# Kernel tuning notes

Measured on AMD Instinct MI355X. Metric: run time of the kernel, lower is better.

## Reference

```python
import jax, jax.numpy as jnp
import numpy as np

EMBED_DIM = 1024

def setup_inputs() -> dict:
    key = jax.random.key(0)
    kx, kq, kk, kv = jax.random.split(key, 4)
    scale = 1.0 / np.sqrt(EMBED_DIM)  # Kaiming-uniform-ish init scale
    x = jax.random.normal(kx, (4, 2048, EMBED_DIM), dtype=jnp.float32)
    Wq = jax.random.uniform(kq, (EMBED_DIM, EMBED_DIM), jnp.float32, -scale, scale)
    Wk = jax.random.uniform(kk, (EMBED_DIM, EMBED_DIM), jnp.float32, -scale, scale)
    Wv = jax.random.uniform(kv, (EMBED_DIM, EMBED_DIM), jnp.float32, -scale, scale)
    return {"x": x, "Wq": Wq, "Wk": Wk, "Wv": Wv}

def reference(x, Wq, Wk, Wv):
    # Linear layers: y = x @ W.T (torch nn.Linear convention, no bias)
    q = jnp.einsum('bsd,ed->bse', x, Wq)
    k = jnp.einsum('bsd,ed->bse', x, Wk)
    v = jnp.einsum('bsd,ed->bse', x, Wv)
    d = k.shape[-1]
    scores = jnp.einsum('bqe,bke->bqk', q, k) / jnp.sqrt(jnp.asarray(d, x.dtype))
    attn = jax.nn.softmax(scores, axis=-1)
    return jnp.einsum('bqk,bke->bqe', attn, v)
```

## Files before the change

### kernel.cpp

```cpp
#include <hip/hip_runtime.h>
#include <hip/hip_bf16.h>

typedef unsigned short u16;
typedef __bf16 bf16x8 __attribute__((ext_vector_type(8)));
typedef float f32x4 __attribute__((ext_vector_type(4)));

__device__ __forceinline__ u16 f2bf(float f) {
    unsigned int u = __builtin_bit_cast(unsigned int, f);
    unsigned int r = u + 0x7FFFu + ((u >> 16) & 1u);
    return (u16)(r >> 16);
}

__device__ __forceinline__ float bf2f(unsigned int bits16) {
    return __builtin_bit_cast(float, bits16 << 16);
}

__device__ __forceinline__ void gload_lds16(const u16* g, u16* l) {
    __builtin_amdgcn_global_load_lds(
        (const __attribute__((address_space(1))) void*)(g),
        (__attribute__((address_space(3))) void*)(l), 16, 0, 0);
}

__global__ __launch_bounds__(256) void cvt_bf16_kernel(
    const float* __restrict__ in, u16* __restrict__ out, int n8)
{
    int i = blockIdx.x * 256 + threadIdx.x;
    if (i >= n8) return;
    const float4* p = (const float4*)in + 2 * (long long)i;
    float4 a = p[0], b = p[1];
    uint4 o;
    o.x = (unsigned)f2bf(a.x) | ((unsigned)f2bf(a.y) << 16);
    o.y = (unsigned)f2bf(a.z) | ((unsigned)f2bf(a.w) << 16);
    o.z = (unsigned)f2bf(b.x) | ((unsigned)f2bf(b.y) << 16);
    o.w = (unsigned)f2bf(b.z) | ((unsigned)f2bf(b.w) << 16);
    ((uint4*)out)[i] = o;
}

__global__ __launch_bounds__(256) void cvt3_bf16_kernel(
    const float* __restrict__ a, const float* __restrict__ b,
    const float* __restrict__ c, u16* __restrict__ out, int n8per)
{
    int i = blockIdx.x * 256 + threadIdx.x;
    if (i >= n8per) return;
    const float* in = (blockIdx.y == 0) ? a : ((blockIdx.y == 1) ? b : c);
    const float4* p = (const float4*)in + 2 * (long long)i;
    float4 va = p[0], vb = p[1];
    uint4 o;
    o.x = (unsigned)f2bf(va.x) | ((unsigned)f2bf(va.y) << 16);
    o.y = (unsigned)f2bf(va.z) | ((unsigned)f2bf(va.w) << 16);
    o.z = (unsigned)f2bf(vb.x) | ((unsigned)f2bf(vb.y) << 16);
    o.w = (unsigned)f2bf(vb.z) | ((unsigned)f2bf(vb.w) << 16);
    ((uint4*)(out + (long long)blockIdx.y * n8per * 8))[i] = o;
}

__global__ __launch_bounds__(256) void inv_rows(
    const float* __restrict__ partial, float* __restrict__ inv, int n)
{
    int i = blockIdx.x * 256 + threadIdx.x;
    if (i >= n) return;
    const float* p = partial + (long long)i * 8;
    float s = 0.f;
#pragma unroll
    for (int k = 0; k < 8; ++k) s += p[k];
    inv[i] = 1.0f / s;
}

template <int BN, bool OUT_F32, int EPI>
__global__ __launch_bounds__(512, 2) void gemm4p(
    const u16* __restrict__ A, const u16* __restrict__ B, void* __restrict__ Cv,
    int lda, int ldb, int ldc, int K,
    long long sAz, long long sBz, long long sCz, int cw, int ch,
    float* __restrict__ aux)
{
    constexpr int WC = (BN == 256) ? 4 : 2;
    constexpr int ROWS = (BN == 256) ? 128 : 64;
    constexpr int MI = ROWS / 16;
    constexpr int MIh = MI / 2;
    constexpr int BLOADS = BN / 64;
    constexpr int BNK = BN * 64;

    extern __shared__ u16 lds[];
    u16* ldsB = lds + 32768;

    const int flat = blockIdx.x + gridDim.x * blockIdx.y;
    const int xcd = flat & 7, jj = flat >> 3;
    const int nCx = gridDim.x / cw;
    const int bx = (xcd % nCx) * cw + jj % cw;
    const int by = (xcd / nCx) * ch + jj / cw;

    const int z = blockIdx.z;
    A += (long long)z * sAz;
    B += (long long)z * sBz;

    const int tid  = threadIdx.x;
    const int lane = tid & 63;
    const int wave = tid >> 6;
    const int wr = wave / WC, wc = wave % WC;
    const int m0 = by << 8, n0 = bx * BN;
    const int NT = K >> 6;

    const u16* gAp[4];
    const u16* gBp[BLOADS];
#pragma unroll
    for (int i = 0; i < 4; ++i) {
        int s = tid + i * 512, row = ((s >> 7) << 4) | (s & 15), g = (s >> 4) & 7;
        gAp[i] = A + (long long)(m0 + row) * lda + g * 8;
    }
#pragma unroll
    for (int i = 0; i < BLOADS; ++i) {
        int s = tid + i * 512, row = ((s >> 7) << 4) | (s & 15), g = (s >> 4) & 7;
        gBp[i] = B + (long long)(n0 + row) * ldb + g * 8;
    }
    auto stA = [&](int kt, int buf, int i) {
        gload_lds16(gAp[i] + (long long)kt * 64, lds + buf * 16384 + (tid + i * 512) * 8);
    };
    auto stB = [&](int kt, int buf, int i) {
        gload_lds16(gBp[i] + (long long)kt * 64, ldsB + buf * BNK + (tid + i * 512) * 8);
    };

    f32x4 acc[MI][4] = {};

#pragma unroll
    for (int i = 0; i < 4; ++i) stA(0, 0, i);
#pragma unroll
    for (int i = 0; i < BLOADS; ++i) stB(0, 0, i);
#pragma unroll
    for (int i = 0; i < 4; ++i) stA(1, 1, i);
#pragma unroll
    for (int i = 0; i < BLOADS; ++i) stB(1, 1, i);
    if constexpr (BN == 256) asm volatile("s_waitcnt vmcnt(8)" ::: "memory");
    else                     asm volatile("s_waitcnt vmcnt(6)" ::: "memory");
    __builtin_amdgcn_s_barrier();

    for (int kt = 0; kt < NT; ++kt) {
        const int cur = kt & 1;
        const u16* sAc = lds  + cur * 16384 + lane * 8;
        const u16* sBc = ldsB + cur * BNK   + lane * 8;
        const bool st = (kt + 2 < NT);

        bf16x8 a[MIh][2], b0[2][2], b1[2][2];

#pragma unroll
        for (int mi = 0; mi < MIh; ++mi)
#pragma unroll
            for (int kk = 0; kk < 2; ++kk)
                a[mi][kk] = *(const bf16x8*)(sAc + ((wr * MI + mi) * 8 + kk * 4) * 128);
#pragma unroll
        for (int ni = 0; ni < 2; ++ni)
#pragma unroll
            for (int kk = 0; kk < 2; ++kk)
                b0[ni][kk] = *(const bf16x8*)(sBc + ((wc * 4 + ni) * 8 + kk * 4) * 128);
        __builtin_amdgcn_s_barrier();
        asm volatile("s_waitcnt lgkmcnt(0)" ::: "memory");
        __builtin_amdgcn_s_setprio(1);
#pragma unroll
        for (int kk = 0; kk < 2; ++kk)
#pragma unroll
            for (int mi = 0; mi < MIh; ++mi)
#pragma unroll
                for (int ni = 0; ni < 2; ++ni)
                    acc[mi][ni] = __builtin_amdgcn_mfma_f32_16x16x32_bf16(
                        a[mi][kk], b0[ni][kk], acc[mi][ni], 0, 0, 0);
        __builtin_amdgcn_s_setprio(0);
        __builtin_amdgcn_s_barrier();

#pragma unroll
        for (int ni = 0; ni < 2; ++ni)
#pragma unroll
            for (int kk = 0; kk < 2; ++kk)
                b1[ni][kk] = *(const bf16x8*)(sBc + ((wc * 4 + 2 + ni) * 8 + kk * 4) * 128);
        if constexpr (BN == 256) {
            if (st) { stA(kt + 2, cur, 0); stA(kt + 2, cur, 2); }
        }
        __builtin_amdgcn_s_barrier();
        asm volatile("s_waitcnt lgkmcnt(0)" ::: "memory");
        __builtin_amdgcn_s_setprio(1);
#pragma unroll
        for (int kk = 0; kk < 2; ++kk)
#pragma unroll
            for (int mi = 0; mi < MIh; ++mi)
#pragma unroll
                for (int ni = 0; ni < 2; ++ni)
                    acc[mi][2 + ni] = __builtin_amdgcn_mfma_f32_16x16x32_bf16(
                        a[mi][kk], b1[ni][kk], acc[mi][2 + ni], 0, 0, 0);
        __builtin_amdgcn_s_setprio(0);
        __builtin_amdgcn_s_barrier();

#pragma unroll
        for (int mi = 0; mi < MIh; ++mi)
#pragma unroll
            for (int kk = 0; kk < 2; ++kk)
                a[mi][kk] = *(const bf16x8*)(sAc + ((wr * MI + MIh + mi) * 8 + kk * 4) * 128);
        if (st) {
            if constexpr (BN == 256) { stB(kt + 2, cur, 0); stB(kt + 2, cur, 1); }
            else                     { stB(kt + 2, cur, 0); }
        }
        __builtin_amdgcn_s_barrier();
        asm volatile("s_waitcnt lgkmcnt(0)" ::: "memory");
        __builtin_amdgcn_s_setprio(1);
#pragma unroll
        for (int kk = 0; kk < 2; ++kk)
#pragma unroll
            for (int mi = 0; mi < MIh; ++mi)
#pragma unroll
                for (int ni = 0; ni < 2; ++ni)
                    acc[MIh + mi][ni] = __builtin_amdgcn_mfma_f32_16x16x32_bf16(
                        a[mi][kk], b0[ni][kk], acc[MIh + mi][ni], 0, 0, 0);
        __builtin_amdgcn_s_setprio(0);
        __builtin_amdgcn_s_barrier();

        if (st) {
            if constexpr (BN == 256) {
                stA(kt + 2, cur, 1); stA(kt + 2, cur, 3);
                stB(kt + 2, cur, 2); stB(kt + 2, cur, 3);
            } else {
                stA(kt + 2, cur, 0); stA(kt + 2, cur, 1);
                stA(kt + 2, cur, 2); stA(kt + 2, cur, 3);
                stB(kt + 2, cur, 1);
            }
        }
        __builtin_amdgcn_s_barrier();
        __builtin_amdgcn_s_setprio(1);
#pragma unroll
        for (int kk = 0; kk < 2; ++kk)
#pragma unroll
            for (int mi = 0; mi < MIh; ++mi)
#pragma unroll
                for (int ni = 0; ni < 2; ++ni)
                    acc[MIh + mi][2 + ni] = __builtin_amdgcn_mfma_f32_16x16x32_bf16(
                        a[mi][kk], b1[ni][kk], acc[MIh + mi][2 + ni], 0, 0, 0);
        __builtin_amdgcn_s_setprio(0);
        if (st) {
            if constexpr (BN == 256) asm volatile("s_waitcnt vmcnt(8)" ::: "memory");
            else                     asm volatile("s_waitcnt vmcnt(6)" ::: "memory");
        } else if (kt + 1 < NT) {
            asm volatile("s_waitcnt vmcnt(0)" ::: "memory");
        }
        __builtin_amdgcn_s_barrier();
    }

    const int fl = lane & 15, fg = lane >> 4;
    const int er0 = m0 + wr * ROWS + fg * 4;
    const int ec0 = n0 + wc * 64 + fl;

    if constexpr (EPI == 1) {
        u16* C = (u16*)Cv + (long long)z * sCz;
        float lsum[MI][4];
#pragma unroll
        for (int mi = 0; mi < MI; ++mi)
#pragma unroll
            for (int j = 0; j < 4; ++j) {
                float s = 0.f;
#pragma unroll
                for (int ni = 0; ni < 4; ++ni) {
                    float e = __expf(acc[mi][ni][j] * 0.03125f);
                    u16 h = f2bf(e);
                    C[(long long)(er0 + mi * 16 + j) * ldc + ec0 + ni * 16] = h;
                    s += bf2f(h);
                }
                lsum[mi][j] = s;
            }
#pragma unroll
        for (int mi = 0; mi < MI; ++mi)
#pragma unroll
            for (int j = 0; j < 4; ++j)
#pragma unroll
                for (int off = 1; off < 16; off <<= 1)
                    lsum[mi][j] += __shfl_xor(lsum[mi][j], off, 64);
        float (*rsbuf)[4] = reinterpret_cast<float(*)[4]>(lds);
        if (fl == 0) {
#pragma unroll
            for (int mi = 0; mi < MI; ++mi)
#pragma unroll
                for (int j = 0; j < 4; ++j)
                    rsbuf[wr * ROWS + mi * 16 + fg * 4 + j][wc] = lsum[mi][j];
        }
        __syncthreads();
        if (tid < 256) {
            float s = rsbuf[tid][0] + rsbuf[tid][1] + rsbuf[tid][2] + rsbuf[tid][3];
            aux[((long long)z * 2048 + m0 + tid) * 8 + bx] = s;
        }
    } else if constexpr (EPI == 2) {
        float* C = (float*)Cv + (long long)z * sCz;
        float iv[MI][4];
#pragma unroll
        for (int mi = 0; mi < MI; ++mi)
#pragma unroll
            for (int j = 0; j < 4; ++j)
                iv[mi][j] = aux[(long long)z * 2048 + er0 + mi * 16 + j];
#pragma unroll
        for (int mi = 0; mi < MI; ++mi)
#pragma unroll
            for (int ni = 0; ni < 4; ++ni)
#pragma unroll
                for (int j = 0; j < 4; ++j)
                    C[(long long)(er0 + mi * 16 + j) * ldc + ec0 + ni * 16] =
                        acc[mi][ni][j] * iv[mi][j];
    } else if constexpr (OUT_F32) {
        float* C = (float*)Cv + (long long)z * sCz;
#pragma unroll
        for (int mi = 0; mi < MI; ++mi)
#pragma unroll
            for (int ni = 0; ni < 4; ++ni)
#pragma unroll
                for (int j = 0; j < 4; ++j)
                    C[(long long)(er0 + mi * 16 + j) * ldc + ec0 + ni * 16] = acc[mi][ni][j];
    } else {
        u16* C = (u16*)Cv + (long long)z * sCz;
#pragma unroll
        for (int mi = 0; mi < MI; ++mi)
#pragma unroll
            for (int ni = 0; ni < 4; ++ni)
#pragma unroll
                for (int j = 0; j < 4; ++j)
                    C[(long long)(er0 + mi * 16 + j) * ldc + ec0 + ni * 16] = f2bf(acc[mi][ni][j]);
    }
}

extern "C" void kernel_launch(void* const* d_in, const int* in_sizes, int n_in,
                              void* d_out, int out_size, void* d_ws, size_t ws_size,
                              hipStream_t stream) {
    const float* x  = (const float*)d_in[0];
    const float* Wq = (const float*)d_in[1];
    const float* Wk = (const float*)d_in[2];
    const float* Wv = (const float*)d_in[3];
    float* out = (float*)d_out;

    const int B = 4, S = 2048, D = 1024;
    const long long MS = (long long)B * S;

    u16* Sc  = (u16*)d_ws;
    u16* xb  = Sc;
    u16* wqk = Sc  + (long long)B * S * S;
    u16* wvb = wqk + 2 * D * D;
    u16* qk  = wvb + D * D;
    u16* vT  = qk  + MS * 2 * D;
    float* partial = (float*)(vT + MS * D);
    float* inv     = partial + (long long)MS * 8;
    size_t need = (size_t)2 * ((long long)B * S * S + 3 * D * D + MS * 2 * D + MS * D)
                + (size_t)4 * (MS * 8 + MS);
    if (ws_size < need) return;

    hipFuncSetAttribute(reinterpret_cast<const void*>(&gemm4p<256, false, 0>),
                        hipFuncAttributeMaxDynamicSharedMemorySize, 131072);
    hipFuncSetAttribute(reinterpret_cast<const void*>(&gemm4p<128, false, 0>),
                        hipFuncAttributeMaxDynamicSharedMemorySize, 98304);
    hipFuncSetAttribute(reinterpret_cast<const void*>(&gemm4p<256, false, 1>),
                        hipFuncAttributeMaxDynamicSharedMemorySize, 131072);
    hipFuncSetAttribute(reinterpret_cast<const void*>(&gemm4p<128, true, 2>),
                        hipFuncAttributeMaxDynamicSharedMemorySize, 98304);

    cvt_bf16_kernel<<<(int)(MS * D / 8 / 256), 256, 0, stream>>>(x, xb, (int)(MS * D / 8));
    cvt3_bf16_kernel<<<dim3(D * D / 8 / 256, 3, 1), 256, 0, stream>>>(
        Wq, Wk, Wv, wqk, D * D / 8);

    gemm4p<256, false, 0><<<dim3(2 * D / 256, (int)(MS / 256), 1), 512, 131072, stream>>>(
        xb, wqk, qk, D, D, 2 * D, D, 0, 0, 0, 8, 4, nullptr);

    gemm4p<128, false, 0><<<dim3((int)(MS / 128), D / 256, 1), 512, 98304, stream>>>(
        wvb, xb, vT, D, D, (int)MS, D, 0, 0, 0, 8, 4, nullptr);

    gemm4p<256, false, 1><<<dim3(S / 256, S / 256, B), 512, 131072, stream>>>(
        qk, qk + D, Sc, 2 * D, 2 * D, S, D,
        (long long)S * 2 * D, (long long)S * 2 * D, (long long)S * S, 2, 4, partial);

    inv_rows<<<(int)(MS / 256), 256, 0, stream>>>(partial, inv, (int)MS);

    gemm4p<128, true, 2><<<dim3(D / 128, S / 256, B), 512, 98304, stream>>>(
        Sc, vT, out, S, (int)MS, D, S,
        (long long)S * S, (long long)S, (long long)S * D, 4, 2, inv);
}
```

Baseline: 182.7 us.

## Add 128x128-tile GEMM kernel for V projection, scores and PV stages

Introduces a new 256-thread gemm4h kernel with 128x128 output tiles and a 4-phase double-buffered LDS pipeline, and uses it for the V projection, the QK^T score/exp stage and the PV stage in place of the larger 512-thread tiles. Row-sum partials now have 16 column blocks per row instead of 8, so inv_rows takes a runtime width. Smaller tiles give more blocks and less LDS per block, aiming at better occupancy and load balance. The cost is lower per-block operand reuse and more global traffic.

```diff
diff --git a/kernel.cpp b/kernel.cpp
--- a/kernel.cpp
+++ b/kernel.cpp
@@ -54,14 +54,13 @@
 }
 
 __global__ __launch_bounds__(256) void inv_rows(
-    const float* __restrict__ partial, float* __restrict__ inv, int n)
+    const float* __restrict__ partial, float* __restrict__ inv, int n, int w)
 {
     int i = blockIdx.x * 256 + threadIdx.x;
     if (i >= n) return;
-    const float* p = partial + (long long)i * 8;
+    const float* p = partial + (long long)i * w;
     float s = 0.f;
-#pragma unroll
-    for (int k = 0; k < 8; ++k) s += p[k];
+    for (int k = 0; k < w; ++k) s += p[k];
     inv[i] = 1.0f / s;
 }
 
@@ -242,12 +241,186 @@
     const int fl = lane & 15, fg = lane >> 4;
     const int er0 = m0 + wr * ROWS + fg * 4;
     const int ec0 = n0 + wc * 64 + fl;
+    if constexpr (OUT_F32) {
+        float* C = (float*)Cv + (long long)z * sCz;
+#pragma unroll
+        for (int mi = 0; mi < MI; ++mi)
+#pragma unroll
+            for (int ni = 0; ni < 4; ++ni)
+#pragma unroll
+                for (int j = 0; j < 4; ++j)
+                    C[(long long)(er0 + mi * 16 + j) * ldc + ec0 + ni * 16] = acc[mi][ni][j];
+    } else {
+        u16* C = (u16*)Cv + (long long)z * sCz;
+#pragma unroll
+        for (int mi = 0; mi < MI; ++mi)
+#pragma unroll
+            for (int ni = 0; ni < 4; ++ni)
+#pragma unroll
+                for (int j = 0; j < 4; ++j)
+                    C[(long long)(er0 + mi * 16 + j) * ldc + ec0 + ni * 16] = f2bf(acc[mi][ni][j]);
+    }
+}
+
+template <int EPI>
+__global__ __launch_bounds__(256, 2) void gemm4h(
+    const u16* __restrict__ A, const u16* __restrict__ B, void* __restrict__ Cv,
+    int lda, int ldb, int ldc, int K,
+    long long sAz, long long sBz, long long sCz, int cw, int ch,
+    float* __restrict__ aux, int PW)
+{
+    extern __shared__ u16 lds[];
+    u16* ldsB = lds + 16384;
+
+    const int flat = blockIdx.x + gridDim.x * blockIdx.y;
+    const int xcd = flat & 7, jj = flat >> 3;
+    const int nCx = gridDim.x / cw;
+    const int bx = (xcd % nCx) * cw + jj % cw;
+    const int by = (xcd / nCx) * ch + jj / cw;
+
+    const int z = blockIdx.z;
+    A += (long long)z * sAz;
+    B += (long long)z * sBz;
+
+    const int tid = threadIdx.x, lane = tid & 63, wave = tid >> 6;
+    const int wr = wave >> 1, wc = wave & 1;
+    const int m0 = by << 7, n0 = bx << 7;
+    const int NT = K >> 6;
+
+    const u16* gAp[4];
+    const u16* gBp[4];
+#pragma unroll
+    for (int i = 0; i < 4; ++i) {
+        int s = tid + i * 256, row = ((s >> 7) << 4) | (s & 15), g = (s >> 4) & 7;
+        gAp[i] = A + (long long)(m0 + row) * lda + g * 8;
+        gBp[i] = B + (long long)(n0 + row) * ldb + g * 8;
+    }
+    auto stA = [&](int kt, int buf, int i) {
+        gload_lds16(gAp[i] + (long long)kt * 64, lds + buf * 8192 + (tid + i * 256) * 8);
+    };
+    auto stB = [&](int kt, int buf, int i) {
+        gload_lds16(gBp[i] + (long long)kt * 64, ldsB + buf * 8192 + (tid + i * 256) * 8);
+    };
+
+    f32x4 acc[4][4] = {};
+
+#pragma unroll
+    for (int i = 0; i < 4; ++i) stA(0, 0, i);
+#pragma unroll
+    for (int i = 0; i < 4; ++i) stB(0, 0, i);
+#pragma unroll
+    for (int i = 0; i < 4; ++i) stA(1, 1, i);
+#pragma unroll
+    for (int i = 0; i < 4; ++i) stB(1, 1, i);
+    asm volatile("s_waitcnt vmcnt(8)" ::: "memory");
+    __builtin_amdgcn_s_barrier();
+
+    const int laneoff = (lane >> 4) * 128 + (lane & 15) * 8;
+
+    for (int kt = 0; kt < NT; ++kt) {
+        const int cur = kt & 1;
+        const u16* sAc = lds  + cur * 8192 + laneoff;
+        const u16* sBc = ldsB + cur * 8192 + laneoff;
+        const bool st = (kt + 2 < NT);
+
+        bf16x8 a[2][2], b0[2][2], b1[2][2];
+
+#pragma unroll
+        for (int mi = 0; mi < 2; ++mi)
+#pragma unroll
+            for (int kk = 0; kk < 2; ++kk)
+                a[mi][kk] = *(const bf16x8*)(sAc + (wr * 4 + mi) * 1024 + kk * 512);
+#pragma unroll
+        for (int ni = 0; ni < 2; ++ni)
+#pragma unroll
+            for (int kk = 0; kk < 2; ++kk)
+                b0[ni][kk] = *(const bf16x8*)(sBc + (wc * 4 + ni) * 1024 + kk * 512);
+        __builtin_amdgcn_s_barrier();
+        asm volatile("s_waitcnt lgkmcnt(0)" ::: "memory");
+        __builtin_amdgcn_s_setprio(1);
+#pragma unroll
+        for (int kk = 0; kk < 2; ++kk)
+#pragma unroll
+            for (int mi = 0; mi < 2; ++mi)
+#pragma unroll
+                for (int ni = 0; ni < 2; ++ni)
+                    acc[mi][ni] = __builtin_amdgcn_mfma_f32_16x16x32_bf16(
+                        a[mi][kk], b0[ni][kk], acc[mi][ni], 0, 0, 0);
+        __builtin_amdgcn_s_setprio(0);
+        __builtin_amdgcn_s_barrier();
+
+#pragma unroll
+        for (int ni = 0; ni < 2; ++ni)
+#pragma unroll
+            for (int kk = 0; kk < 2; ++kk)
+                b1[ni][kk] = *(const bf16x8*)(sBc + (wc * 4 + 2 + ni) * 1024 + kk * 512);
+        if (st) { stA(kt + 2, cur, 0); stA(kt + 2, cur, 2); }
+        __builtin_amdgcn_s_barrier();
+        asm volatile("s_waitcnt lgkmcnt(0)" ::: "memory");
+        __builtin_amdgcn_s_setprio(1);
+#pragma unroll
+        for (int kk = 0; kk < 2; ++kk)
+#pragma unroll
+            for (int mi = 0; mi < 2; ++mi)
+#pragma unroll
+                for (int ni = 0; ni < 2; ++ni)
+                    acc[mi][2 + ni] = __builtin_amdgcn_mfma_f32_16x16x32_bf16(
+                        a[mi][kk], b1[ni][kk], acc[mi][2 + ni], 0, 0, 0);
+        __builtin_amdgcn_s_setprio(0);
+        __builtin_amdgcn_s_barrier();
+
+#pragma unroll
+        for (int mi = 0; mi < 2; ++mi)
+#pragma unroll
+            for (int kk = 0; kk < 2; ++kk)
+                a[mi][kk] = *(const bf16x8*)(sAc + (wr * 4 + 2 + mi) * 1024 + kk * 512);
+        if (st) { stB(kt + 2, cur, 0); stB(kt + 2, cur, 1); }
+        __builtin_amdgcn_s_barrier();
+        asm volatile("s_waitcnt lgkmcnt(0)" ::: "memory");
+        __builtin_amdgcn_s_setprio(1);
+#pragma unroll
+        for (int kk = 0; kk < 2; ++kk)
+#pragma unroll
+            for (int mi = 0; mi < 2; ++mi)
+#pragma unroll
+                for (int ni = 0; ni < 2; ++ni)
+                    acc[2 + mi][ni] = __builtin_amdgcn_mfma_f32_16x16x32_bf16(
+                        a[mi][kk], b0[ni][kk], acc[2 + mi][ni], 0, 0, 0);
+        __builtin_amdgcn_s_setprio(0);
+        __builtin_amdgcn_s_barrier();
+
+        if (st) {
+            stA(kt + 2, cur, 1); stA(kt + 2, cur, 3);
+            stB(kt + 2, cur, 2); stB(kt + 2, cur, 3);
+        }
+        __builtin_amdgcn_s_barrier();
+        __builtin_amdgcn_s_setprio(1);
+#pragma unroll
+        for (int kk = 0; kk < 2; ++kk)
+#pragma unroll
+            for (int mi = 0; mi < 2; ++mi)
+#pragma unroll
+                for (int ni = 0; ni < 2; ++ni)
+                    acc[2 + mi][2 + ni] = __builtin_amdgcn_mfma_f32_16x16x32_bf16(
+                        a[mi][kk], b1[ni][kk], acc[2 + mi][2 + ni], 0, 0, 0);
+        __builtin_amdgcn_s_setprio(0);
+        if (st) {
+            asm volatile("s_waitcnt vmcnt(8)" ::: "memory");
+        } else if (kt + 1 < NT) {
+            asm volatile("s_waitcnt vmcnt(0)" ::: "memory");
+        }
+        __builtin_amdgcn_s_barrier();
+    }
+
+    const int fl = lane & 15, fg = lane >> 4;
+    const int er0 = m0 + wr * 64 + fg * 4;
+    const int ec0 = n0 + wc * 64 + fl;
 
     if constexpr (EPI == 1) {
         u16* C = (u16*)Cv + (long long)z * sCz;
-        float lsum[MI][4];
-#pragma unroll
-        for (int mi = 0; mi < MI; ++mi)
+        float lsum[4][4];
+#pragma unroll
+        for (int mi = 0; mi < 4; ++mi)
 #pragma unroll
             for (int j = 0; j < 4; ++j) {
                 float s = 0.f;
@@ -261,54 +434,43 @@
                 lsum[mi][j] = s;
             }
 #pragma unroll
-        for (int mi = 0; mi < MI; ++mi)
+        for (int mi = 0; mi < 4; ++mi)
 #pragma unroll
             for (int j = 0; j < 4; ++j)
 #pragma unroll
                 for (int off = 1; off < 16; off <<= 1)
                     lsum[mi][j] += __shfl_xor(lsum[mi][j], off, 64);
-        float (*rsbuf)[4] = reinterpret_cast<float(*)[4]>(lds);
+        float (*rsbuf)[2] = reinterpret_cast<float(*)[2]>(lds);
         if (fl == 0) {
 #pragma unroll
-            for (int mi = 0; mi < MI; ++mi)
+            for (int mi = 0; mi < 4; ++mi)
 #pragma unroll
                 for (int j = 0; j < 4; ++j)
-                    rsbuf[wr * ROWS + mi * 16 + fg * 4 + j][wc] = lsum[mi][j];
+                    rsbuf[wr * 64 + mi * 16 + fg * 4 + j][wc] = lsum[mi][j];
         }
         __syncthreads();
-        if (tid < 256) {
-            float s = rsbuf[tid][0] + rsbuf[tid][1] + rsbuf[tid][2] + rsbuf[tid][3];
-            aux[((long long)z * 2048 + m0 + tid) * 8 + bx] = s;
-        }
+        if (tid < 128)
+            aux[((long long)z * 2048 + m0 + tid) * PW + bx] = rsbuf[tid][0] + rsbuf[tid][1];
     } else if constexpr (EPI == 2) {
         float* C = (float*)Cv + (long long)z * sCz;
-        float iv[MI][4];
-#pragma unroll
-        for (int mi = 0; mi < MI; ++mi)
+        float iv[4][4];
+#pragma unroll
+        for (int mi = 0; mi < 4; ++mi)
 #pragma unroll
             for (int j = 0; j < 4; ++j)
                 iv[mi][j] = aux[(long long)z * 2048 + er0 + mi * 16 + j];
 #pragma unroll
-        for (int mi = 0; mi < MI; ++mi)
+        for (int mi = 0; mi < 4; ++mi)
 #pragma unroll
             for (int ni = 0; ni < 4; ++ni)
 #pragma unroll
                 for (int j = 0; j < 4; ++j)
                     C[(long long)(er0 + mi * 16 + j) * ldc + ec0 + ni * 16] =
                         acc[mi][ni][j] * iv[mi][j];
-    } else if constexpr (OUT_F32) {
-        float* C = (float*)Cv + (long long)z * sCz;
-#pragma unroll
-        for (int mi = 0; mi < MI; ++mi)
-#pragma unroll
-            for (int ni = 0; ni < 4; ++ni)
-#pragma unroll
-                for (int j = 0; j < 4; ++j)
-                    C[(long long)(er0 + mi * 16 + j) * ldc + ec0 + ni * 16] = acc[mi][ni][j];
     } else {
         u16* C = (u16*)Cv + (long long)z * sCz;
 #pragma unroll
-        for (int mi = 0; mi < MI; ++mi)
+        for (int mi = 0; mi < 4; ++mi)
 #pragma unroll
             for (int ni = 0; ni < 4; ++ni)
 #pragma unroll
@@ -336,19 +498,19 @@
     u16* qk  = wvb + D * D;
     u16* vT  = qk  + MS * 2 * D;
     float* partial = (float*)(vT + MS * D);
-    float* inv     = partial + (long long)MS * 8;
+    float* inv     = partial + (long long)MS * 16;
     size_t need = (size_t)2 * ((long long)B * S * S + 3 * D * D + MS * 2 * D + MS * D)
-                + (size_t)4 * (MS * 8 + MS);
+                + (size_t)4 * (MS * 16 + MS);
     if (ws_size < need) return;
 
     hipFuncSetAttribute(reinterpret_cast<const void*>(&gemm4p<256, false, 0>),
                         hipFuncAttributeMaxDynamicSharedMemorySize, 131072);
-    hipFuncSetAttribute(reinterpret_cast<const void*>(&gemm4p<128, false, 0>),
-                        hipFuncAttributeMaxDynamicSharedMemorySize, 98304);
-    hipFuncSetAttribute(reinterpret_cast<const void*>(&gemm4p<256, false, 1>),
-                        hipFuncAttributeMaxDynamicSharedMemorySize, 131072);
-    hipFuncSetAttribute(reinterpret_cast<const void*>(&gemm4p<128, true, 2>),
-                        hipFuncAttributeMaxDynamicSharedMemorySize, 98304);
+    hipFuncSetAttribute(reinterpret_cast<const void*>(&gemm4h<0>),
+                        hipFuncAttributeMaxDynamicSharedMemorySize, 65536);
+    hipFuncSetAttribute(reinterpret_cast<const void*>(&gemm4h<1>),
+                        hipFuncAttributeMaxDynamicSharedMemorySize, 65536);
+    hipFuncSetAttribute(reinterpret_cast<const void*>(&gemm4h<2>),
+                        hipFuncAttributeMaxDynamicSharedMemorySize, 65536);
 
     cvt_bf16_kernel<<<(int)(MS * D / 8 / 256), 256, 0, stream>>>(x, xb, (int)(MS * D / 8));
     cvt3_bf16_kernel<<<dim3(D * D / 8 / 256, 3, 1), 256, 0, stream>>>(
@@ -357,16 +519,16 @@
     gemm4p<256, false, 0><<<dim3(2 * D / 256, (int)(MS / 256), 1), 512, 131072, stream>>>(
         xb, wqk, qk, D, D, 2 * D, D, 0, 0, 0, 8, 4, nullptr);
 
-    gemm4p<128, false, 0><<<dim3((int)(MS / 128), D / 256, 1), 512, 98304, stream>>>(
-        wvb, xb, vT, D, D, (int)MS, D, 0, 0, 0, 8, 4, nullptr);
-
-    gemm4p<256, false, 1><<<dim3(S / 256, S / 256, B), 512, 131072, stream>>>(
+    gemm4h<0><<<dim3((int)(MS / 128), D / 128, 1), 256, 65536, stream>>>(
+        wvb, xb, vT, D, D, (int)MS, D, 0, 0, 0, 8, 8, nullptr, 0);
+
+    gemm4h<1><<<dim3(S / 128, S / 128, B), 256, 65536, stream>>>(
         qk, qk + D, Sc, 2 * D, 2 * D, S, D,
-        (long long)S * 2 * D, (long long)S * 2 * D, (long long)S * S, 2, 4, partial);
-
-    inv_rows<<<(int)(MS / 256), 256, 0, stream>>>(partial, inv, (int)MS);
-
-    gemm4p<128, true, 2><<<dim3(D / 128, S / 256, B), 512, 98304, stream>>>(
+        (long long)S * 2 * D, (long long)S * 2 * D, (long long)S * S, 4, 8, partial, 16);
+
+    inv_rows<<<(int)(MS / 256), 256, 0, stream>>>(partial, inv, (int)MS, 16);
+
+    gemm4h<2><<<dim3(D / 128, S / 128, B), 256, 65536, stream>>>(
         Sc, vT, out, S, (int)MS, D, S,
-        (long long)S * S, (long long)S, (long long)S * D, 4, 2, inv);
-}
+        (long long)S * S, (long long)S, (long long)S * D, 4, 4, inv, 0);
+}
```

New measurement: 220.1 us. 20.5% more time.
